# Optimization experiments

Hardware: AMD Instinct MI355X
Metric: run time of the kernel (lower is better)

Reference implementation:

```python
import jax, jax.numpy as jnp
import numpy as np

B, T, C, HS = 1024, 128, 384, 64


def setup_inputs() -> dict:
    key = jax.random.key(0)
    k1, k2, k3, k4 = jax.random.split(key, 4)
    std = 1.0 / np.sqrt(C)  # ~ nn.Linear default init scale
    return {
        "x": jax.random.normal(k1, (B, T, C), dtype=jnp.float32),
        "Wq": jax.random.normal(k2, (C, HS), dtype=jnp.float32) * std,
        "Wk": jax.random.normal(k3, (C, HS), dtype=jnp.float32) * std,
        "Wv": jax.random.normal(k4, (C, HS), dtype=jnp.float32) * std,
    }


def reference(x, Wq, Wk, Wv):
    # x: [B, T, C]; Wq/Wk/Wv: [C, HS]
    q = jnp.einsum("btc,ch->bth", x, Wq)
    k = jnp.einsum("btc,ch->bth", x, Wk)
    v = jnp.einsum("btc,ch->bth", x, Wv)
    scale = 1.0 / jnp.sqrt(jnp.asarray(k.shape[-1], dtype=x.dtype))
    wei = jnp.einsum("bth,bsh->bts", q, k) * scale  # [B, T, T]
    t = x.shape[1]
    causal = jnp.tril(jnp.ones((t, t), dtype=bool))
    wei = jnp.where(causal, wei, jnp.asarray(-jnp.inf, dtype=wei.dtype))
    wei = jax.nn.softmax(wei, axis=-1)
    # dropout omitted (eval mode / deterministic reference)
    out = jnp.einsum("bts,bsh->bth", wei, v)  # [B, T, HS]
    return out
```

## Files before the change

### kernel.cpp

```cpp
#include <hip/hip_runtime.h>


typedef __attribute__((ext_vector_type(8)))  short  short8;
typedef __attribute__((ext_vector_type(16))) float  floatx16;
typedef __attribute__((ext_vector_type(4)))  float  float4v;

#define T_DIM   128
#define C_DIM   384
#define HS      64
#define NCHUNK  12
#define SLAB    1536

#define QK_PITCH 68
#define V_PITCH  132
#define P_PITCH  132
#define Q_OFF 0
#define K_OFF 17408
#define V_OFF 34816
#define LDS_BYTES 51712
#define P_OFF 0

#define MFMA(a,b,c) __builtin_amdgcn_mfma_f32_32x32x16_bf16((a),(b),(c),0,0,0)

__device__ inline unsigned short f2bf(float f){
    unsigned u = __builtin_bit_cast(unsigned, f);
    u += 0x7FFFu + ((u >> 16) & 1u);
    return (unsigned short)(u >> 16);
}

__device__ inline short8 ld_b64x2(const char* p){
    union { unsigned long long u[2]; short8 s; } r;
    r.u[0] = *(const unsigned long long*)(p);
    r.u[1] = *(const unsigned long long*)(p + 8);
    return r.s;
}

__global__ void prep_wt(const float* __restrict__ Wq, const float* __restrict__ Wk,
                        const float* __restrict__ Wv, unsigned short* __restrict__ wt){
    int idx = blockIdx.x * 256 + threadIdx.x;
    if (idx >= 48 * SLAB) return;
    int slab = idx / SLAB;
    int rem  = idx - slab * SLAB;
    int n = rem >> 3, j = rem & 7;
    int half = slab & 1, ks = (slab >> 1) & 1, c = slab >> 2;
    int kg = c*32 + ks*16 + half*8 + j;
    const float* W = (n < 64) ? Wq : (n < 128) ? Wk : Wv;
    wt[idx] = f2bf(W[kg * HS + (n & 63)]);
}

__launch_bounds__(256, 2)
__global__ void attn_kernel(const float* __restrict__ x,
                            const unsigned short* __restrict__ wtg,
                            float* __restrict__ out){
    __shared__ __align__(16) char smem[LDS_BYTES];
    const int tid  = threadIdx.x;
    const int lane = tid & 63;
    const int wave = tid >> 6;
    const int l31  = lane & 31;
    const int half = lane >> 5;
    const int koff = half * 8;
    const int b    = blockIdx.x;
    const float* xb = x + (size_t)b * (T_DIM * C_DIM);

    const int mpair = wave & 1;
    const int ntri  = wave >> 1;
    const int mrow0 = 64 * mpair + l31;
    const short8* wf = (const short8*)wtg;
    const int nbase = 96 * ntri + l31;

    floatx16 acc[6] = {};
    float4v bufA[8], bufB[8];

    auto xload = [&](float4v (&buf)[8], int c){
        #pragma unroll
        for (int ks = 0; ks < 2; ++ks)
            #pragma unroll
            for (int mbl = 0; mbl < 2; ++mbl){
                const float* g = xb + (mrow0 + 32*mbl)*C_DIM + (c*32 + ks*16 + koff);
                buf[ks*4+mbl*2+0] = *(const float4v*)g;
                buf[ks*4+mbl*2+1] = *(const float4v*)(g + 4);
            }
    };
    auto body = [&](int c, float4v (&cur)[8], float4v (&nxt)[8]){
        if (c + 1 < NCHUNK) xload(nxt, c + 1);
        short8 afrag[2][2];
        #pragma unroll
        for (int ks = 0; ks < 2; ++ks)
            #pragma unroll
            for (int mbl = 0; mbl < 2; ++mbl){
                float4v lo = cur[ks*4+mbl*2+0], hi = cur[ks*4+mbl*2+1];
                short8 a;
                a[0]=(short)f2bf(lo[0]); a[1]=(short)f2bf(lo[1]);
                a[2]=(short)f2bf(lo[2]); a[3]=(short)f2bf(lo[3]);
                a[4]=(short)f2bf(hi[0]); a[5]=(short)f2bf(hi[1]);
                a[6]=(short)f2bf(hi[2]); a[7]=(short)f2bf(hi[3]);
                afrag[ks][mbl] = a;
            }
        #pragma unroll
        for (int ks = 0; ks < 2; ++ks){
            const short8* slab = wf + ((c*2 + ks)*2 + half) * 192;
            #pragma unroll
            for (int nbl = 0; nbl < 3; ++nbl){
                short8 bfrag = slab[nbase + 32*nbl];
                acc[nbl*2+0] = MFMA(afrag[ks][0], bfrag, acc[nbl*2+0]);
                acc[nbl*2+1] = MFMA(afrag[ks][1], bfrag, acc[nbl*2+1]);
            }
        }
    };

    xload(bufA, 0);
    for (int cc = 0; cc < NCHUNK; cc += 2){
        body(cc,     bufA, bufB);
        body(cc + 1, bufB, bufA);
    }

    const float QSCALE = 0.125f * 1.44269504088896f;
    #pragma unroll
    for (int nbl = 0; nbl < 3; ++nbl)
        #pragma unroll
        for (int mbl = 0; mbl < 2; ++mbl){
            floatx16 A = acc[nbl*2+mbl];
            int nb = 3*ntri + nbl;
            int mb = 2*mpair + mbl;
            if (nb < 4){
                int base  = (nb < 2) ? Q_OFF : K_OFF;
                int col   = 32 * (nb & 1) + l31;
                float sc  = (nb < 2) ? QSCALE : 1.0f;
                char* bp  = smem + base + col * 2;
                #pragma unroll
                for (int r = 0; r < 16; ++r){
                    int t = 32*mb + (r&3) + 8*(r>>2) + 4*half;
                    *(unsigned short*)(bp + t * (QK_PITCH*2)) = f2bf(A[r] * sc);
                }
            } else {
                int h = 32*(nb-4) + l31;
                char* bp = smem + V_OFF + h * (V_PITCH*2);
                #pragma unroll
                for (int g = 0; g < 4; ++g){
                    int t0 = 32*mb + 8*g + 4*half;
                    union { unsigned short s[4]; unsigned long long u; } pk;
                    pk.s[0]=f2bf(A[4*g+0]); pk.s[1]=f2bf(A[4*g+1]);
                    pk.s[2]=f2bf(A[4*g+2]); pk.s[3]=f2bf(A[4*g+3]);
                    *(unsigned long long*)(bp + t0*2) = pk.u;
                }
            }
        }
    __syncthreads();

    floatx16 accS[4] = {};
    #pragma unroll
    for (int ks = 0; ks < 4; ++ks){
        short8 aq = ld_b64x2(smem + Q_OFF + (32*wave + l31)*(QK_PITCH*2) + (ks*16 + koff)*2);
        #pragma unroll
        for (int st = 0; st < 4; ++st)
            if (st <= wave){
                short8 bk = ld_b64x2(smem + K_OFF + (32*st + l31)*(QK_PITCH*2) + (ks*16 + koff)*2);
                accS[st] = MFMA(aq, bk, accS[st]);
            }
    }
    #pragma unroll
    for (int st = 0; st < 4; ++st)
        if (st <= wave){
            #pragma unroll
            for (int r = 0; r < 16; ++r){
                int trow = (r&3) + 8*(r>>2) + 4*half;
                float e = exp2f(accS[st][r]);
                if (st == wave && l31 > trow) e = 0.0f;
                accS[st][r] = e;
            }
        }

    float linv[16];
    #pragma unroll
    for (int r = 0; r < 16; ++r){
        float l = accS[0][r] + accS[1][r] + accS[2][r] + accS[3][r];
        #pragma unroll
        for (int m = 1; m <= 16; m <<= 1)
            l += __shfl_xor(l, m);
        linv[r] = 1.0f / l;
    }
    __syncthreads();

    #pragma unroll
    for (int st = 0; st < 4; ++st)
        if (st <= wave){
            char* bp = smem + P_OFF + (32*st + l31) * 2;
            #pragma unroll
            for (int r = 0; r < 16; ++r){
                int t = 32*wave + (r&3) + 8*(r>>2) + 4*half;
                *(unsigned short*)(bp + t * (P_PITCH*2)) = f2bf(accS[st][r]);
            }
        }
    __syncthreads();

    floatx16 accO0 = {}, accO1 = {};
    const int nks = 2 * (wave + 1);
    #pragma unroll
    for (int ks = 0; ks < 8; ++ks)
        if (ks < nks){
            short8 ap  = ld_b64x2(smem + P_OFF + (32*wave + l31)*(P_PITCH*2) + (ks*16 + koff)*2);
            short8 bv0 = ld_b64x2(smem + V_OFF + l31        *(V_PITCH*2) + (ks*16 + koff)*2);
            short8 bv1 = ld_b64x2(smem + V_OFF + (l31 + 32) *(V_PITCH*2) + (ks*16 + koff)*2);
            accO0 = MFMA(ap, bv0, accO0);
            accO1 = MFMA(ap, bv1, accO1);
        }

    float* ob = out + (size_t)b * (T_DIM * HS);
    #pragma unroll
    for (int r = 0; r < 16; ++r){
        int t = 32*wave + (r&3) + 8*(r>>2) + 4*half;
        ob[t*HS + l31]      = accO0[r] * linv[r];
        ob[t*HS + l31 + 32] = accO1[r] * linv[r];
    }
}

extern "C" void kernel_launch(void* const* d_in, const int* in_sizes, int n_in,
                              void* d_out, int out_size, void* d_ws, size_t ws_size,
                              hipStream_t stream){
    const float* x  = (const float*)d_in[0];
    const float* Wq = (const float*)d_in[1];
    const float* Wk = (const float*)d_in[2];
    const float* Wv = (const float*)d_in[3];
    unsigned short* wt = (unsigned short*)d_ws;

    prep_wt<<<288, 256, 0, stream>>>(Wq, Wk, Wv, wt);
    attn_kernel<<<1024, 256, 0, stream>>>(x, wt, (float*)d_out);
}
```

Baseline: 315.4 us.

## Stage x chunks into LDS via async global_load_lds with swizzle, raise occupancy

The x tile is no longer read straight from global memory into a register double buffer. Each chunk is now copied into a double-buffered, XOR-swizzled LDS region with global_load_lds, then read back as fragments and converted to bf16. This frees the register buffers so launch bounds can request 3 blocks per SM, and the async copy is meant to overlap the next chunk's load with the current MFMAs. In exchange it adds a block barrier on every chunk and reuses the Q/K LDS region, which relies on the final sync before the projection epilogue.

```diff
diff --git a/kernel.cpp b/kernel.cpp
--- a/kernel.cpp
+++ b/kernel.cpp
@@ -19,6 +19,8 @@
 #define V_OFF 34816
 #define LDS_BYTES 51712
 #define P_OFF 0
+#define XS_OFF 0
+#define XS_BUF 16384
 
 #define MFMA(a,b,c) __builtin_amdgcn_mfma_f32_32x32x16_bf16((a),(b),(c),0,0,0)
 
@@ -48,7 +50,7 @@
     wt[idx] = f2bf(W[kg * HS + (n & 63)]);
 }
 
-__launch_bounds__(256, 2)
+__launch_bounds__(256, 3)
 __global__ void attn_kernel(const float* __restrict__ x,
                             const unsigned short* __restrict__ wtg,
                             float* __restrict__ out){
@@ -64,55 +66,70 @@
 
     const int mpair = wave & 1;
     const int ntri  = wave >> 1;
-    const int mrow0 = 64 * mpair + l31;
     const short8* wf = (const short8*)wtg;
     const int nbase = 96 * ntri + l31;
 
+    const char* xsrc = (const char*)xb
+                     + (lane >> 3) * (C_DIM * 4)
+                     + ((((lane & 7) ^ (lane >> 3))) << 4);
+
+    auto stage = [&](int c, int sb){
+        #pragma unroll
+        for (int i = 0; i < 4; ++i){
+            const char* g = xsrc + (i*4 + wave) * (8 * C_DIM * 4) + c * 128;
+            char*       l = smem + XS_OFF + sb * XS_BUF + (i*4 + wave) * 1024;
+            __builtin_amdgcn_global_load_lds(
+                (const __attribute__((address_space(1))) unsigned*)g,
+                (__attribute__((address_space(3))) unsigned*)l,
+                16, 0, 0);
+        }
+    };
+
     floatx16 acc[6] = {};
-    float4v bufA[8], bufB[8];
-
-    auto xload = [&](float4v (&buf)[8], int c){
+    stage(0, 0);
+
+    #pragma unroll
+    for (int c = 0; c < NCHUNK; ++c){
+        __syncthreads();
+
+        short8 bfr[2][3];
         #pragma unroll
         for (int ks = 0; ks < 2; ++ks)
             #pragma unroll
-            for (int mbl = 0; mbl < 2; ++mbl){
-                const float* g = xb + (mrow0 + 32*mbl)*C_DIM + (c*32 + ks*16 + koff);
-                buf[ks*4+mbl*2+0] = *(const float4v*)g;
-                buf[ks*4+mbl*2+1] = *(const float4v*)(g + 4);
-            }
-    };
-    auto body = [&](int c, float4v (&cur)[8], float4v (&nxt)[8]){
-        if (c + 1 < NCHUNK) xload(nxt, c + 1);
-        short8 afrag[2][2];
-        #pragma unroll
-        for (int ks = 0; ks < 2; ++ks)
-            #pragma unroll
-            for (int mbl = 0; mbl < 2; ++mbl){
-                float4v lo = cur[ks*4+mbl*2+0], hi = cur[ks*4+mbl*2+1];
+            for (int nbl = 0; nbl < 3; ++nbl)
+                bfr[ks][nbl] = wf[((c*2 + ks)*2 + half)*192 + nbase + 32*nbl];
+
+        if (c + 1 < NCHUNK) stage(c + 1, (c + 1) & 1);
+
+        const char* sbuf = smem + XS_OFF + (c & 1) * XS_BUF;
+        short8 afr[2][2];
+        #pragma unroll
+        for (int mbl = 0; mbl < 2; ++mbl){
+            const int R  = 64*mpair + 32*mbl + l31;
+            const char* rp = sbuf + R * 128;
+            const int sw = (R & 7) << 4;
+            #pragma unroll
+            for (int ks = 0; ks < 2; ++ks){
+                const int cb = ks*64 + half*32;
+                float4v lo = *(const float4v*)(rp + ((cb     ) ^ sw));
+                float4v hi = *(const float4v*)(rp + ((cb + 16) ^ sw));
                 short8 a;
                 a[0]=(short)f2bf(lo[0]); a[1]=(short)f2bf(lo[1]);
                 a[2]=(short)f2bf(lo[2]); a[3]=(short)f2bf(lo[3]);
                 a[4]=(short)f2bf(hi[0]); a[5]=(short)f2bf(hi[1]);
                 a[6]=(short)f2bf(hi[2]); a[7]=(short)f2bf(hi[3]);
-                afrag[ks][mbl] = a;
-            }
-        #pragma unroll
-        for (int ks = 0; ks < 2; ++ks){
-            const short8* slab = wf + ((c*2 + ks)*2 + half) * 192;
+                afr[ks][mbl] = a;
+            }
+        }
+        #pragma unroll
+        for (int ks = 0; ks < 2; ++ks)
             #pragma unroll
             for (int nbl = 0; nbl < 3; ++nbl){
-                short8 bfrag = slab[nbase + 32*nbl];
-                acc[nbl*2+0] = MFMA(afrag[ks][0], bfrag, acc[nbl*2+0]);
-                acc[nbl*2+1] = MFMA(afrag[ks][1], bfrag, acc[nbl*2+1]);
-            }
-        }
-    };
-
-    xload(bufA, 0);
-    for (int cc = 0; cc < NCHUNK; cc += 2){
-        body(cc,     bufA, bufB);
-        body(cc + 1, bufB, bufA);
-    }
+                acc[nbl*2+0] = MFMA(afr[ks][0], bfr[ks][nbl], acc[nbl*2+0]);
+                acc[nbl*2+1] = MFMA(afr[ks][1], bfr[ks][nbl], acc[nbl*2+1]);
+            }
+    }
+    __syncthreads();
 
     const float QSCALE = 0.125f * 1.44269504088896f;
     #pragma unroll
```

Result: no change. 311.2 us (-1.3%).
